# Kernel tuning notes

Hardware: AMD Instinct MI355X
Metric: run time of the kernel (lower is better)

The kernel has to match this reference:

```python
import jax, jax.numpy as jnp
import numpy as np

NUM_ROIS = 200  # Schaefer200: labels 1..200, 0 = background


def setup_inputs() -> dict:
    key = jax.random.key(0)
    k1, k2 = jax.random.split(key)
    B, C, D, H, W = 4, 256, 46, 55, 46
    feature_map = jax.random.normal(k1, (B, C, D, H, W), dtype=jnp.float32)
    # atlas already at the feature-map resolution (nearest resample is identity here)
    atlas = jax.random.randint(k2, (D, H, W), 0, NUM_ROIS + 1, dtype=jnp.int32)
    return {"feature_map": feature_map, "atlas": atlas}


def reference(feature_map, atlas):
    B, C, D, H, W = feature_map.shape
    N = D * H * W
    seg = atlas.reshape(N)                      # int labels in [0, NUM_ROIS]
    feats = feature_map.reshape(B, C, N)
    # single-pass segment mean keyed by atlas label (segment 0 = background)
    sums = jax.ops.segment_sum(
        jnp.transpose(feats, (2, 0, 1)),        # (N, B, C)
        seg, num_segments=NUM_ROIS + 1)         # (NUM_ROIS+1, B, C)
    counts = jax.ops.segment_sum(
        jnp.ones((N,), dtype=feature_map.dtype), seg,
        num_segments=NUM_ROIS + 1)              # (NUM_ROIS+1,)
    roi_sums = jnp.transpose(sums, (1, 0, 2))[:, 1:, :]   # (B, NUM_ROIS, C)
    roi_counts = counts[1:]                                # (NUM_ROIS,)
    valid = roi_counts > 0                                 # (NUM_ROIS,)
    denom = jnp.where(valid, roi_counts, 1.0)[None, :, None]
    roi_features = jnp.where(valid[None, :, None], roi_sums / denom, 0.0)
    roi_valid_mask = jnp.broadcast_to(valid[None, :], (B, NUM_ROIS))
    return roi_features, roi_valid_mask
```

## Files before the change

kernel.cpp:

```cpp
#include <hip/hip_runtime.h>

#define NB 4
#define NC 256
#define NN 116380
#define NVEC (NN/4)
#define NR 200
#define NL 201
#define NPLANES (NB*NC)
#define NFEAT (NB*NR*NC)
#define MROI 256
#define CHV 64
#define NCH 1818
#define NTAIL 28
#define AOFFD 4096
#define BUFD 4160
#define NBUF 3

typedef __attribute__((ext_vector_type(8))) short bf16x8;
typedef __attribute__((ext_vector_type(4))) float f32x4;

union BU { uint4 u; bf16x8 v; };

__device__ __forceinline__ unsigned pkbf(float x, float y) {
    unsigned ux = __float_as_uint(x) + 0x8000u;
    unsigned uy = __float_as_uint(y) + 0x8000u;
    return __builtin_amdgcn_perm(uy, ux, 0x07060302u);
}
__device__ __forceinline__ unsigned oh2(int l0, int l1, int c) {
    return (l0 == c ? 0x3F80u : 0u) | (l1 == c ? 0x3F800000u : 0u);
}
__device__ __forceinline__ bf16x8 mkA(const int4& la, const int4& lb, int c) {
    union { unsigned u[4]; bf16x8 v; } x;
    x.u[0] = oh2(la.x, la.y, c);
    x.u[1] = oh2(la.z, la.w, c);
    x.u[2] = oh2(lb.x, lb.y, c);
    x.u[3] = oh2(lb.z, lb.w, c);
    return x.v;
}

__global__ __launch_bounds__(256) void roi_count(const int* __restrict__ atlas,
                                                 float* __restrict__ counts) {
    __shared__ float h[NL];
    const int tid = threadIdx.x;
    for (int i = tid; i < NL; i += 256) h[i] = 0.0f;
    __syncthreads();
    const int iv = blockIdx.x * 256 + tid;
    if (iv < NVEC) {
        int4 lab = ((const int4*)atlas)[iv];
        atomicAdd(&h[lab.x], 1.0f);
        atomicAdd(&h[lab.y], 1.0f);
        atomicAdd(&h[lab.z], 1.0f);
        atomicAdd(&h[lab.w], 1.0f);
    }
    __syncthreads();
    for (int i = tid; i < NL; i += 256) {
        float v = h[i];
        if (i > 0 && v != 0.0f) atomicAdd(&counts[i - 1], v);
    }
}

__global__ __launch_bounds__(256, 3) void roi_accum_async(const float* __restrict__ fm,
                                                          const int* __restrict__ atlas,
                                                          float* __restrict__ partials) {
    __shared__ unsigned lds[NBUF * BUFD];
    const int tid  = threadIdx.x;
    const int wave = tid >> 6;
    const int lane = tid & 63;
    const int g    = lane >> 4;
    const int n    = lane & 15;
    const int pb   = blockIdx.y * 64;
    const int x    = blockIdx.x;
    const int gx   = gridDim.x;

    const int base = NCH / gx, rem = NCH % gx;
    const int c0 = x * base + min(x, rem);
    const int c1 = c0 + base + (x < rem ? 1 : 0);

    f32x4 acc[4][4];
    #pragma unroll
    for (int t = 0; t < 4; ++t)
        #pragma unroll
        for (int p = 0; p < 4; ++p)
            acc[t][p] = (f32x4){0.f, 0.f, 0.f, 0.f};

    const int t0    = wave * 4;
    const int cbase = t0 * 16 + n + 1;
    const int NT    = (wave == 3) ? 1 : 4;

    auto STAGE = [&](int ch, int b) {
        #pragma unroll
        for (int j = 0; j < 4; ++j) {
            const int row  = wave * 16 + j * 4 + (lane >> 4);
            const int colp = (lane & 15) * 4;
            const int col  = colp ^ ((row & 7) << 2);
            const float* gp = fm + (size_t)(pb + row) * NN + ch * CHV + col;
            unsigned* lp = &lds[b * BUFD + (wave * 4 + j) * 256];
            __builtin_amdgcn_global_load_lds(
                (const __attribute__((address_space(1))) unsigned*)gp,
                (__attribute__((address_space(3))) unsigned*)lp, 16, 0, 0);
        }
        const int* ga = atlas + ch * CHV + lane;
        __builtin_amdgcn_global_load_lds(
            (const __attribute__((address_space(1))) unsigned*)ga,
            (__attribute__((address_space(3))) unsigned*)&lds[b * BUFD + AOFFD], 4, 0, 0);
    };

    auto CONSUME_KS = [&](int b, int ks) {
        const unsigned* ap = &lds[b * BUFD + AOFFD + ks * 32 + 8 * g];
        int4 la = *(const int4*)ap;
        int4 lb = *(const int4*)(ap + 4);
        BU Bp[4];
        #pragma unroll
        for (int p = 0; p < 4; ++p) {
            const int row = p * 16 + n;
            const int xr  = (row & 7) << 2;
            const int cb  = ks * 32 + g * 8;
            f32x4 f0 = *(const f32x4*)&lds[b * BUFD + row * 64 + (cb ^ xr)];
            f32x4 f1 = *(const f32x4*)&lds[b * BUFD + row * 64 + ((cb + 4) ^ xr)];
            Bp[p].u = make_uint4(pkbf(f0[0], f0[1]), pkbf(f0[2], f0[3]),
                                 pkbf(f1[0], f1[1]), pkbf(f1[2], f1[3]));
        }
        #pragma unroll
        for (int t = 0; t < 4; ++t) {
            if (t < NT) {
                bf16x8 A = mkA(la, lb, cbase + 16 * t);
                acc[t][0] = __builtin_amdgcn_mfma_f32_16x16x32_bf16(A, Bp[0].v, acc[t][0], 0, 0, 0);
                acc[t][1] = __builtin_amdgcn_mfma_f32_16x16x32_bf16(A, Bp[1].v, acc[t][1], 0, 0, 0);
                acc[t][2] = __builtin_amdgcn_mfma_f32_16x16x32_bf16(A, Bp[2].v, acc[t][2], 0, 0, 0);
                acc[t][3] = __builtin_amdgcn_mfma_f32_16x16x32_bf16(A, Bp[3].v, acc[t][3], 0, 0, 0);
            }
        }
    };

    if (c0 + 0 < c1) STAGE(c0 + 0, 0);
    if (c0 + 1 < c1) STAGE(c0 + 1, 1);
    if (c0 + 2 < c1) STAGE(c0 + 2, 2);

    int b = 0;
    for (int c = c0; c < c1; ++c) {
        const int ahead = min(c1, c + 3) - (c + 1);
        if (ahead >= 2)      asm volatile("s_waitcnt vmcnt(10)" ::: "memory");
        else if (ahead == 1) asm volatile("s_waitcnt vmcnt(5)" ::: "memory");
        else                 asm volatile("s_waitcnt vmcnt(0)" ::: "memory");
        __builtin_amdgcn_s_barrier();
        __builtin_amdgcn_sched_barrier(0);
        CONSUME_KS(b, 0);
        CONSUME_KS(b, 1);
        __builtin_amdgcn_sched_barrier(0);
        __builtin_amdgcn_s_barrier();
        if (c + 3 < c1) STAGE(c + 3, b);
        b = (b == 2) ? 0 : b + 1;
    }

    if (c1 == NCH && c0 < c1) {
        const int row = tid >> 2, scq = tid & 3;
        #pragma unroll
        for (int i = 0; i < 8; ++i) {
            const int cl = scq * 8 + i;
            float v = (cl < NTAIL) ? fm[(size_t)(pb + row) * NN + NCH * CHV + cl] : 0.0f;
            lds[row * 64 + (cl ^ ((row & 7) << 2))] = __float_as_uint(v);
        }
        if (tid < CHV) {
            int a = (tid < NTAIL) ? atlas[NCH * CHV + tid] : 0;
            lds[AOFFD + tid] = (unsigned)a;
        }
        __syncthreads();
        CONSUME_KS(0, 0);
    }

    float* pc = partials + (size_t)x * (MROI * NPLANES);
    const int rbase = 4 * g;
    #pragma unroll
    for (int t = 0; t < 4; ++t) {
        if (t < NT) {
            #pragma unroll
            for (int p = 0; p < 4; ++p)
                #pragma unroll
                for (int i = 0; i < 4; ++i)
                    pc[(size_t)((t0 + t) * 16 + rbase + i) * NPLANES + (pb + 16 * p + n)] = acc[t][p][i];
        }
    }
}

__global__ __launch_bounds__(256) void roi_final2(const float* __restrict__ partials,
                                                  const float* __restrict__ counts,
                                                  float* __restrict__ out,
                                                  const int kch) {
    const int j = blockIdx.x * 256 + threadIdx.x;
    if (j < NFEAT) {
        const int c = j & (NC - 1);
        const int r = (j >> 8) % NR;
        const int bb = j / (NR * NC);
        const int plane = bb * NC + c;
        float s = 0.0f;
        for (int ch = 0; ch < kch; ++ch)
            s += partials[((size_t)ch * MROI + r) * NPLANES + plane];
        const float cnt = counts[r];
        out[j] = (cnt > 0.0f) ? s / cnt : 0.0f;
    } else if (j < NFEAT + NB * NR) {
        const int r = (j - NFEAT) % NR;
        out[j] = (counts[r] > 0.0f) ? 1.0f : 0.0f;
    }
}

extern "C" void kernel_launch(void* const* d_in, const int* in_sizes, int n_in,
                              void* d_out, int out_size, void* d_ws, size_t ws_size,
                              hipStream_t stream) {
    const float* fm    = (const float*)d_in[0];
    const int*   atlas = (const int*)d_in[1];
    float*       out   = (float*)d_out;

    float* counts   = (float*)d_ws;
    float* partials = counts + 256;

    int kch = 48;
    while (kch > 12 &&
           ws_size < 1024 + (size_t)kch * MROI * NPLANES * sizeof(float))
        kch >>= 1;

    hipMemsetAsync(counts, 0, NR * sizeof(float), stream);

    roi_count<<<(NVEC + 255) / 256, 256, 0, stream>>>(atlas, counts);

    roi_accum_async<<<dim3(kch, 16), 256, 0, stream>>>(fm, atlas, partials);

    const int total = NFEAT + NB * NR;
    roi_final2<<<(total + 255) / 256, 256, 0, stream>>>(partials, counts, out, kch);
}
```

Measured before the change: 134.9 us.

## Widen accum tile to 128 planes per block with double buffering

Each block now covers 128 feature planes instead of 64, so every one-hot A fragment built from the atlas labels is reused across 8 B tiles, and the label loads and one-hot work per plane are halved. The LDS ring drops from three to two buffers to make room for the larger tile, and occupancy falls to 2 blocks per CU. The grid gets 64 chunk splits instead of 48, which raises the partials workspace and the reduction work in the final kernel. The shallower prefetch and heavier register use (accumulators double) could expose more memory latency.

```diff
diff --git a/kernel.cpp b/kernel.cpp
--- a/kernel.cpp
+++ b/kernel.cpp
@@ -12,9 +12,10 @@
 #define CHV 64
 #define NCH 1818
 #define NTAIL 28
-#define AOFFD 4096
-#define BUFD 4160
-#define NBUF 3
+#define PPB 128
+#define AOFFD (PPB*64)
+#define BUFD (AOFFD + 64)
+#define NBUF 2
 
 typedef __attribute__((ext_vector_type(8))) short bf16x8;
 typedef __attribute__((ext_vector_type(4))) float f32x4;
@@ -59,16 +60,16 @@
     }
 }
 
-__global__ __launch_bounds__(256, 3) void roi_accum_async(const float* __restrict__ fm,
-                                                          const int* __restrict__ atlas,
-                                                          float* __restrict__ partials) {
+__global__ __launch_bounds__(256, 2) void roi_accum_w(const float* __restrict__ fm,
+                                                      const int* __restrict__ atlas,
+                                                      float* __restrict__ partials) {
     __shared__ unsigned lds[NBUF * BUFD];
     const int tid  = threadIdx.x;
     const int wave = tid >> 6;
     const int lane = tid & 63;
     const int g    = lane >> 4;
     const int n    = lane & 15;
-    const int pb   = blockIdx.y * 64;
+    const int pb   = blockIdx.y * PPB;
     const int x    = blockIdx.x;
     const int gx   = gridDim.x;
 
@@ -76,11 +77,11 @@
     const int c0 = x * base + min(x, rem);
     const int c1 = c0 + base + (x < rem ? 1 : 0);
 
-    f32x4 acc[4][4];
+    f32x4 acc[4][8];
     #pragma unroll
     for (int t = 0; t < 4; ++t)
         #pragma unroll
-        for (int p = 0; p < 4; ++p)
+        for (int p = 0; p < 8; ++p)
             acc[t][p] = (f32x4){0.f, 0.f, 0.f, 0.f};
 
     const int t0    = wave * 4;
@@ -89,12 +90,12 @@
 
     auto STAGE = [&](int ch, int b) {
         #pragma unroll
-        for (int j = 0; j < 4; ++j) {
-            const int row  = wave * 16 + j * 4 + (lane >> 4);
+        for (int j = 0; j < 8; ++j) {
+            const int row  = (wave * 8 + j) * 4 + (lane >> 4);
             const int colp = (lane & 15) * 4;
             const int col  = colp ^ ((row & 7) << 2);
             const float* gp = fm + (size_t)(pb + row) * NN + ch * CHV + col;
-            unsigned* lp = &lds[b * BUFD + (wave * 4 + j) * 256];
+            unsigned* lp = &lds[b * BUFD + (wave * 8 + j) * 256];
             __builtin_amdgcn_global_load_lds(
                 (const __attribute__((address_space(1))) unsigned*)gp,
                 (__attribute__((address_space(3))) unsigned*)lp, 16, 0, 0);
@@ -109,56 +110,56 @@
         const unsigned* ap = &lds[b * BUFD + AOFFD + ks * 32 + 8 * g];
         int4 la = *(const int4*)ap;
         int4 lb = *(const int4*)(ap + 4);
-        BU Bp[4];
-        #pragma unroll
-        for (int p = 0; p < 4; ++p) {
+        bf16x8 A0 = mkA(la, lb, cbase);
+        bf16x8 A1 = mkA(la, lb, cbase + 16);
+        bf16x8 A2 = mkA(la, lb, cbase + 32);
+        bf16x8 A3 = mkA(la, lb, cbase + 48);
+        #pragma unroll
+        for (int p = 0; p < 8; ++p) {
             const int row = p * 16 + n;
             const int xr  = (row & 7) << 2;
             const int cb  = ks * 32 + g * 8;
             f32x4 f0 = *(const f32x4*)&lds[b * BUFD + row * 64 + (cb ^ xr)];
             f32x4 f1 = *(const f32x4*)&lds[b * BUFD + row * 64 + ((cb + 4) ^ xr)];
-            Bp[p].u = make_uint4(pkbf(f0[0], f0[1]), pkbf(f0[2], f0[3]),
-                                 pkbf(f1[0], f1[1]), pkbf(f1[2], f1[3]));
-        }
-        #pragma unroll
-        for (int t = 0; t < 4; ++t) {
-            if (t < NT) {
-                bf16x8 A = mkA(la, lb, cbase + 16 * t);
-                acc[t][0] = __builtin_amdgcn_mfma_f32_16x16x32_bf16(A, Bp[0].v, acc[t][0], 0, 0, 0);
-                acc[t][1] = __builtin_amdgcn_mfma_f32_16x16x32_bf16(A, Bp[1].v, acc[t][1], 0, 0, 0);
-                acc[t][2] = __builtin_amdgcn_mfma_f32_16x16x32_bf16(A, Bp[2].v, acc[t][2], 0, 0, 0);
-                acc[t][3] = __builtin_amdgcn_mfma_f32_16x16x32_bf16(A, Bp[3].v, acc[t][3], 0, 0, 0);
+            BU B;
+            B.u = make_uint4(pkbf(f0[0], f0[1]), pkbf(f0[2], f0[3]),
+                             pkbf(f1[0], f1[1]), pkbf(f1[2], f1[3]));
+            acc[0][p] = __builtin_amdgcn_mfma_f32_16x16x32_bf16(A0, B.v, acc[0][p], 0, 0, 0);
+            if (NT > 1) {
+                acc[1][p] = __builtin_amdgcn_mfma_f32_16x16x32_bf16(A1, B.v, acc[1][p], 0, 0, 0);
+                acc[2][p] = __builtin_amdgcn_mfma_f32_16x16x32_bf16(A2, B.v, acc[2][p], 0, 0, 0);
+                acc[3][p] = __builtin_amdgcn_mfma_f32_16x16x32_bf16(A3, B.v, acc[3][p], 0, 0, 0);
             }
         }
     };
 
     if (c0 + 0 < c1) STAGE(c0 + 0, 0);
     if (c0 + 1 < c1) STAGE(c0 + 1, 1);
-    if (c0 + 2 < c1) STAGE(c0 + 2, 2);
 
     int b = 0;
     for (int c = c0; c < c1; ++c) {
-        const int ahead = min(c1, c + 3) - (c + 1);
-        if (ahead >= 2)      asm volatile("s_waitcnt vmcnt(10)" ::: "memory");
-        else if (ahead == 1) asm volatile("s_waitcnt vmcnt(5)" ::: "memory");
-        else                 asm volatile("s_waitcnt vmcnt(0)" ::: "memory");
+        const int ahead = min(c1, c + 2) - (c + 1);
+        if (ahead >= 1) asm volatile("s_waitcnt vmcnt(9)" ::: "memory");
+        else            asm volatile("s_waitcnt vmcnt(0)" ::: "memory");
         __builtin_amdgcn_s_barrier();
         __builtin_amdgcn_sched_barrier(0);
         CONSUME_KS(b, 0);
         CONSUME_KS(b, 1);
         __builtin_amdgcn_sched_barrier(0);
         __builtin_amdgcn_s_barrier();
-        if (c + 3 < c1) STAGE(c + 3, b);
-        b = (b == 2) ? 0 : b + 1;
+        if (c + 2 < c1) STAGE(c + 2, b);
+        b ^= 1;
     }
 
     if (c1 == NCH && c0 < c1) {
-        const int row = tid >> 2, scq = tid & 3;
-        #pragma unroll
-        for (int i = 0; i < 8; ++i) {
-            const int cl = scq * 8 + i;
+        const int row = tid >> 1;
+        const int hh  = tid & 1;
+        const int xr  = (row & 7) << 2;
+        #pragma unroll
+        for (int i = 0; i < 16; ++i) {
+            const int cl = hh * 16 + i;
             float v = (cl < NTAIL) ? fm[(size_t)(pb + row) * NN + NCH * CHV + cl] : 0.0f;
-            lds[row * 64 + (cl ^ ((row & 7) << 2))] = __float_as_uint(v);
+            lds[row * 64 + (cl ^ xr)] = __float_as_uint(v);
         }
         if (tid < CHV) {
             int a = (tid < NTAIL) ? atlas[NCH * CHV + tid] : 0;
@@ -174,7 +175,7 @@
     for (int t = 0; t < 4; ++t) {
         if (t < NT) {
             #pragma unroll
-            for (int p = 0; p < 4; ++p)
+            for (int p = 0; p < 8; ++p)
                 #pragma unroll
                 for (int i = 0; i < 4; ++i)
                     pc[(size_t)((t0 + t) * 16 + rbase + i) * NPLANES + (pb + 16 * p + n)] = acc[t][p][i];
@@ -213,8 +214,8 @@
     float* counts   = (float*)d_ws;
     float* partials = counts + 256;
 
-    int kch = 48;
-    while (kch > 12 &&
+    int kch = 64;
+    while (kch > 16 &&
            ws_size < 1024 + (size_t)kch * MROI * NPLANES * sizeof(float))
         kch >>= 1;
 
@@ -222,7 +223,7 @@
 
     roi_count<<<(NVEC + 255) / 256, 256, 0, stream>>>(atlas, counts);
 
-    roi_accum_async<<<dim3(kch, 16), 256, 0, stream>>>(fm, atlas, partials);
+    roi_accum_w<<<dim3(kch, NPLANES / PPB), 256, 0, stream>>>(fm, atlas, partials);
 
     const int total = NFEAT + NB * NR;
     roi_final2<<<(total + 255) / 256, 256, 0, stream>>>(partials, counts, out, kch);
```

Result: slower. 150.5 us (+11.5%).

## Fuse ROI counting into accumulation kernel and store partials as bf16

Applied to the files above, without the earlier changes.

Removes the separate label-count kernel and computes the per-ROI histogram inside the accumulation kernel, using only the blockIdx.y==0 blocks over each block's chunk range. Partial sums are now stored as bf16 instead of fp32, and the partial-row stride is cut from 256 to 208 ROIs, which shrinks both the workspace writes and the reads in the final reduction. The cost is extra rounding error, since each partial sum is truncated to bf16 before the cross-chunk sum. The y==0 blocks also do more work, which may leave them as stragglers.

```diff
diff --git a/kernel.cpp b/kernel.cpp
--- a/kernel.cpp
+++ b/kernel.cpp
@@ -8,7 +8,7 @@
 #define NL 201
 #define NPLANES (NB*NC)
 #define NFEAT (NB*NR*NC)
-#define MROI 256
+#define MROI 208
 #define CHV 64
 #define NCH 1818
 #define NTAIL 28
@@ -25,6 +25,9 @@
     unsigned ux = __float_as_uint(x) + 0x8000u;
     unsigned uy = __float_as_uint(y) + 0x8000u;
     return __builtin_amdgcn_perm(uy, ux, 0x07060302u);
+}
+__device__ __forceinline__ unsigned short bf1(float x) {
+    return (unsigned short)((__float_as_uint(x) + 0x8000u) >> 16);
 }
 __device__ __forceinline__ unsigned oh2(int l0, int l1, int c) {
     return (l0 == c ? 0x3F80u : 0u) | (l1 == c ? 0x3F800000u : 0u);
@@ -38,30 +41,10 @@
     return x.v;
 }
 
-__global__ __launch_bounds__(256) void roi_count(const int* __restrict__ atlas,
-                                                 float* __restrict__ counts) {
-    __shared__ float h[NL];
-    const int tid = threadIdx.x;
-    for (int i = tid; i < NL; i += 256) h[i] = 0.0f;
-    __syncthreads();
-    const int iv = blockIdx.x * 256 + tid;
-    if (iv < NVEC) {
-        int4 lab = ((const int4*)atlas)[iv];
-        atomicAdd(&h[lab.x], 1.0f);
-        atomicAdd(&h[lab.y], 1.0f);
-        atomicAdd(&h[lab.z], 1.0f);
-        atomicAdd(&h[lab.w], 1.0f);
-    }
-    __syncthreads();
-    for (int i = tid; i < NL; i += 256) {
-        float v = h[i];
-        if (i > 0 && v != 0.0f) atomicAdd(&counts[i - 1], v);
-    }
-}
-
-__global__ __launch_bounds__(256, 3) void roi_accum_async(const float* __restrict__ fm,
-                                                          const int* __restrict__ atlas,
-                                                          float* __restrict__ partials) {
+__global__ __launch_bounds__(256, 3) void roi_accum_f(const float* __restrict__ fm,
+                                                      const int* __restrict__ atlas,
+                                                      unsigned short* __restrict__ partials,
+                                                      float* __restrict__ counts) {
     __shared__ unsigned lds[NBUF * BUFD];
     const int tid  = threadIdx.x;
     const int wave = tid >> 6;
@@ -168,7 +151,7 @@
         CONSUME_KS(0, 0);
     }
 
-    float* pc = partials + (size_t)x * (MROI * NPLANES);
+    unsigned short* pc = partials + (size_t)x * (MROI * NPLANES);
     const int rbase = 4 * g;
     #pragma unroll
     for (int t = 0; t < 4; ++t) {
@@ -177,12 +160,34 @@
             for (int p = 0; p < 4; ++p)
                 #pragma unroll
                 for (int i = 0; i < 4; ++i)
-                    pc[(size_t)((t0 + t) * 16 + rbase + i) * NPLANES + (pb + 16 * p + n)] = acc[t][p][i];
-        }
-    }
-}
-
-__global__ __launch_bounds__(256) void roi_final2(const float* __restrict__ partials,
+                    pc[(size_t)((t0 + t) * 16 + rbase + i) * NPLANES + (pb + 16 * p + n)] = bf1(acc[t][p][i]);
+        }
+    }
+
+    if (blockIdx.y == 0) {
+        float* h = (float*)lds;
+        __syncthreads();
+        for (int i = tid; i < NL; i += 256) h[i] = 0.0f;
+        __syncthreads();
+        const int4* at4b = (const int4*)atlas;
+        for (int i = c0 * 16 + tid; i < c1 * 16; i += 256) {
+            int4 l = at4b[i];
+            atomicAdd(&h[l.x], 1.0f);
+            atomicAdd(&h[l.y], 1.0f);
+            atomicAdd(&h[l.z], 1.0f);
+            atomicAdd(&h[l.w], 1.0f);
+        }
+        if (c1 == NCH && tid < NTAIL)
+            atomicAdd(&h[atlas[NCH * CHV + tid]], 1.0f);
+        __syncthreads();
+        for (int i = 1 + tid; i < NL; i += 256) {
+            float v = h[i];
+            if (v != 0.0f) atomicAdd(&counts[i - 1], v);
+        }
+    }
+}
+
+__global__ __launch_bounds__(256) void roi_final3(const unsigned short* __restrict__ partials,
                                                   const float* __restrict__ counts,
                                                   float* __restrict__ out,
                                                   const int kch) {
@@ -193,8 +198,10 @@
         const int bb = j / (NR * NC);
         const int plane = bb * NC + c;
         float s = 0.0f;
-        for (int ch = 0; ch < kch; ++ch)
-            s += partials[((size_t)ch * MROI + r) * NPLANES + plane];
+        for (int ch = 0; ch < kch; ++ch) {
+            unsigned u = partials[((size_t)ch * MROI + r) * NPLANES + plane];
+            s += __uint_as_float(u << 16);
+        }
         const float cnt = counts[r];
         out[j] = (cnt > 0.0f) ? s / cnt : 0.0f;
     } else if (j < NFEAT + NB * NR) {
@@ -210,20 +217,18 @@
     const int*   atlas = (const int*)d_in[1];
     float*       out   = (float*)d_out;
 
-    float* counts   = (float*)d_ws;
-    float* partials = counts + 256;
+    float*          counts   = (float*)d_ws;
+    unsigned short* partials = (unsigned short*)(counts + 256);
 
     int kch = 48;
     while (kch > 12 &&
-           ws_size < 1024 + (size_t)kch * MROI * NPLANES * sizeof(float))
+           ws_size < 1024 + (size_t)kch * MROI * NPLANES * sizeof(unsigned short))
         kch >>= 1;
 
     hipMemsetAsync(counts, 0, NR * sizeof(float), stream);
 
-    roi_count<<<(NVEC + 255) / 256, 256, 0, stream>>>(atlas, counts);
-
-    roi_accum_async<<<dim3(kch, 16), 256, 0, stream>>>(fm, atlas, partials);
+    roi_accum_f<<<dim3(kch, 16), 256, 0, stream>>>(fm, atlas, partials, counts);
 
     const int total = NFEAT + NB * NR;
-    roi_final2<<<(total + 255) / 256, 256, 0, stream>>>(partials, counts, out, kch);
-}
+    roi_final3<<<(total + 255) / 256, 256, 0, stream>>>(partials, counts, out, kch);
+}
```

Result: faster. 126.2 us (-6.5%).
